# Optimization experiments

Measured on AMD Instinct MI355X. Metric: run time of the kernel, lower is better.

Reference implementation:

```python
import jax, jax.numpy as jnp
import numpy as np

# dims matching init_kwargs
B, N = 1, 2048
VOCAB, DIM, DEPTH = 32000, 1024, 4
HEADS, DIM_HEAD, WINDOW = 16, 64, 512
INNER = HEADS * DIM_HEAD          # 1024
FF_INNER = int(DIM * 4 * 2 / 3)   # 2730 (GEGLU inner)
DPB_DIM = DIM // 2
LN_EPS = 1e-5


def layernorm(x, g, b):
    m = jnp.mean(x, axis=-1, keepdims=True)
    v = jnp.mean(jnp.square(x - m), axis=-1, keepdims=True)
    return (x - m) * jax.lax.rsqrt(v + LN_EPS) * g + b


def look_around(x, backward=1, forward=0, pad_value=-1):
    # x: [b, nw, w, ...]; concat shifted windows along the window_size axis
    nw = x.shape[1]
    pads = [(0, 0), (backward, forward)] + [(0, 0)] * (x.ndim - 2)
    px = jnp.pad(x, pads, constant_values=pad_value)
    return jnp.concatenate([px[:, i:i + nw] for i in range(backward + forward + 1)], axis=2)


def dynamic_pos_bias(w1, b1, w2, b2, w3, b3, i, j):
    # MLP over scalar relative distances, then gather into [H, i, j]
    rel = jnp.arange(j, dtype=jnp.float32)[:, None]            # [j, 1]
    h = jax.nn.silu(rel @ w1 + b1)
    h = jax.nn.silu(h @ w2 + b2)
    bias = h @ w3 + b3                                          # [j, H]
    idx = jnp.abs(jnp.arange(j - i, j)[:, None] - jnp.arange(j)[None, :])  # [i, j]
    return jnp.transpose(bias[idx], (2, 0, 1))                  # [H, i, j]


def local_attention(q, k, v, attn_bias):
    # causal sliding-window attention, look_backward=1, look_forward=0, exact_windowsize=True
    # q,k,v: [B,H,N,dh]; N assumed multiple of WINDOW (autopad is a no-op then)
    b, h, n, d = q.shape
    w = WINDOW
    nw = n // w
    scale = d ** -0.5
    bq = q.reshape(b * h, nw, w, d) * scale
    bk = look_around(k.reshape(b * h, nw, w, d), pad_value=-1.0)   # [bh,nw,2w,d]
    bv = look_around(v.reshape(b * h, nw, w, d), pad_value=-1.0)
    t = jnp.arange(n).reshape(1, nw, w)
    bq_t = t[..., :, None]                                      # [1,nw,w,1]
    bq_k = look_around(t, pad_value=-1)[..., None, :]           # [1,nw,1,2w]
    # causal | exact-window | padding masks
    mask = (bq_t < bq_k) | (bq_t > bq_k + w) | (bq_k == -1)
    sim = jnp.einsum('bwid,bwjd->bwij', bq, bk)                 # [bh,nw,w,2w]
    sim = (sim.reshape(b, h, nw, w, 2 * w) + attn_bias[None, :, None]).reshape(b * h, nw, w, 2 * w)
    sim = jnp.where(mask, -jnp.finfo(sim.dtype).max, sim)
    attn = jax.nn.softmax(sim, axis=-1)
    out = jnp.einsum('bwij,bwjd->bwid', attn, bv)
    return out.reshape(b, h, n, d)


def forward(tokens, tok_emb, pos_emb, dpb_w1, dpb_b1, dpb_w2, dpb_b2, dpb_w3, dpb_b3,
            ln1_g, ln1_b, Wqkv, Wo, ln2_g, ln2_b, Wff1, Wff2, lnf_g, lnf_b, Wlogits):
    bsz, n = tokens.shape
    x = tok_emb[tokens] + pos_emb[:n]                           # [B,N,D]
    bias = dynamic_pos_bias(dpb_w1, dpb_b1, dpb_w2, dpb_b2, dpb_w3, dpb_b3, WINDOW, 2 * WINDOW)

    def split_heads(t):
        return t.reshape(bsz, n, HEADS, DIM_HEAD).transpose(0, 2, 1, 3)

    for l in range(DEPTH):
        # LocalMHA (prenorm) + residual
        h = layernorm(x, ln1_g[l], ln1_b[l])
        q, k, v = jnp.split(h @ Wqkv[l], 3, axis=-1)
        o = local_attention(split_heads(q), split_heads(k), split_heads(v), bias)
        o = o.transpose(0, 2, 1, 3).reshape(bsz, n, INNER)
        x = x + o @ Wo[l]
        # GEGLU FFN (prenorm inside FeedForward) + residual
        h = layernorm(x, ln2_g[l], ln2_b[l])
        a, gate = jnp.split(h @ Wff1[l], 2, axis=-1)
        x = x + (a * jax.nn.gelu(gate, approximate=False)) @ Wff2[l]

    return layernorm(x, lnf_g, lnf_b) @ Wlogits                 # [B,N,V]


def setup_inputs() -> dict:
    key = jax.random.key(0)
    ks = iter(jax.random.split(key, 16))
    s = 0.02
    rn = lambda *shape: jax.random.normal(next(ks), shape, dtype=jnp.float32) * s
    return {
        'tokens': jax.random.randint(next(ks), (B, N), 0, VOCAB, dtype=jnp.int32),
        'tok_emb': rn(VOCAB, DIM),
        'pos_emb': rn(N, DIM),
        'dpb_w1': rn(1, DPB_DIM), 'dpb_b1': jnp.zeros((DPB_DIM,), jnp.float32),
        'dpb_w2': rn(DPB_DIM, DPB_DIM), 'dpb_b2': jnp.zeros((DPB_DIM,), jnp.float32),
        'dpb_w3': rn(DPB_DIM, HEADS), 'dpb_b3': jnp.zeros((HEADS,), jnp.float32),
        'ln1_g': jnp.ones((DEPTH, DIM), jnp.float32), 'ln1_b': jnp.zeros((DEPTH, DIM), jnp.float32),
        'Wqkv': rn(DEPTH, DIM, 3 * INNER),
        'Wo': rn(DEPTH, INNER, DIM),
        'ln2_g': jnp.ones((DEPTH, DIM), jnp.float32), 'ln2_b': jnp.zeros((DEPTH, DIM), jnp.float32),
        'Wff1': rn(DEPTH, DIM, 2 * FF_INNER),
        'Wff2': rn(DEPTH, FF_INNER, DIM),
        'lnf_g': jnp.ones((DIM,), jnp.float32), 'lnf_b': jnp.zeros((DIM,), jnp.float32),
        'Wlogits': rn(DIM, VOCAB),
    }


def reference(tokens, tok_emb, pos_emb, dpb_w1, dpb_b1, dpb_w2, dpb_b2, dpb_w3, dpb_b3,
              ln1_g, ln1_b, Wqkv, Wo, ln2_g, ln2_b, Wff1, Wff2, lnf_g, lnf_b, Wlogits):
    return forward(tokens, tok_emb, pos_emb, dpb_w1, dpb_b1, dpb_w2, dpb_b2, dpb_w3, dpb_b3,
                   ln1_g, ln1_b, Wqkv, Wo, ln2_g, ln2_b, Wff1, Wff2, lnf_g, lnf_b, Wlogits)
```

## Files before the change

### kernel.cpp

```cpp
#include <hip/hip_runtime.h>
#include <cstdint>

#define DEV __device__ __forceinline__

typedef __attribute__((ext_vector_type(8))) short bf16x8;
typedef __attribute__((ext_vector_type(4))) short bf16x4;
typedef __attribute__((ext_vector_type(4))) float f32x4;

DEV float bf2f(unsigned short u) { return __uint_as_float(((unsigned)u) << 16); }
DEV unsigned short f2bf(float f) {
  unsigned u = __float_as_uint(f);
  u += 0x7FFFu + ((u >> 16) & 1u);
  return (unsigned short)(u >> 16);
}

DEV void gload_lds16(const void* g, void* lds) {
  __builtin_amdgcn_global_load_lds(
      (const __attribute__((address_space(1))) unsigned int*)g,
      (__attribute__((address_space(3))) unsigned int*)lds, 16, 0, 0);
}

__global__ __launch_bounds__(256) void k_embed(const int* __restrict__ tokens,
    const float* __restrict__ tok_emb, const float* __restrict__ pos_emb,
    float* __restrict__ x) {
  int n = blockIdx.x;
  int tok = tokens[n];
  int c = threadIdx.x * 4;
  float4 a = *(const float4*)(tok_emb + (long)tok * 1024 + c);
  float4 p = *(const float4*)(pos_emb + (long)n * 1024 + c);
  float4 r;
  r.x = a.x + p.x; r.y = a.y + p.y; r.z = a.z + p.z; r.w = a.w + p.w;
  *(float4*)(x + (long)n * 1024 + c) = r;
}

__global__ __launch_bounds__(256) void k_ln(const float* __restrict__ x,
    const float* __restrict__ g, const float* __restrict__ b,
    unsigned short* __restrict__ out) {
  __shared__ float red[8];
  int row = blockIdx.x, t = threadIdx.x;
  const float* xr = x + (long)row * 1024;
  float4 v = *(const float4*)(xr + t * 4);
  float s = v.x + v.y + v.z + v.w;
#pragma unroll
  for (int off = 32; off; off >>= 1) s += __shfl_xor(s, off);
  if ((t & 63) == 0) red[t >> 6] = s;
  __syncthreads();
  float mean = (red[0] + red[1] + red[2] + red[3]) * (1.0f / 1024.0f);
  float dx = v.x - mean, dy = v.y - mean, dz = v.z - mean, dw = v.w - mean;
  float sq = dx * dx + dy * dy + dz * dz + dw * dw;
#pragma unroll
  for (int off = 32; off; off >>= 1) sq += __shfl_xor(sq, off);
  if ((t & 63) == 0) red[4 + (t >> 6)] = sq;
  __syncthreads();
  float var = (red[4] + red[5] + red[6] + red[7]) * (1.0f / 1024.0f);
  float inv = rsqrtf(var + 1e-5f);
  int c = t * 4;
  float4 gv = *(const float4*)(g + c);
  float4 bv = *(const float4*)(b + c);
  ushort4 o;
  o.x = f2bf(dx * inv * gv.x + bv.x);
  o.y = f2bf(dy * inv * gv.y + bv.y);
  o.z = f2bf(dz * inv * gv.z + bv.z);
  o.w = f2bf(dw * inv * gv.w + bv.w);
  *(ushort4*)(out + (long)row * 1024 + c) = o;
}

__global__ __launch_bounds__(256) void k_wconv(const float* __restrict__ src,
    unsigned short* __restrict__ dst, int K, int N, int Kp, int Np,
    long sstride, long dstride) {
  __shared__ float tile[32][33];
  const float* s = src + (long)blockIdx.z * sstride;
  unsigned short* d = dst + (long)blockIdx.z * dstride;
  int n0 = blockIdx.x * 32, k0 = blockIdx.y * 32;
  int t = threadIdx.x;
  int r = t >> 3, c4 = (t & 7) * 4;
  int k = k0 + r;
#pragma unroll
  for (int e = 0; e < 4; ++e) {
    int n = n0 + c4 + e;
    tile[r][c4 + e] = (k < K && n < N) ? s[(long)k * N + n] : 0.0f;
  }
  __syncthreads();
  int nrow = n0 + r;
  ushort4 o;
  o.x = f2bf(tile[c4 + 0][r]);
  o.y = f2bf(tile[c4 + 1][r]);
  o.z = f2bf(tile[c4 + 2][r]);
  o.w = f2bf(tile[c4 + 3][r]);
  (void)Np;
  *(ushort4*)(d + (long)nrow * Kp + k0 + c4) = o;
}

__global__ __launch_bounds__(256) void k_dpb(const float* __restrict__ w1,
    const float* __restrict__ b1, const float* __restrict__ w2,
    const float* __restrict__ b2, const float* __restrict__ w3,
    const float* __restrict__ b3, float* __restrict__ table) {
  __shared__ float h1[512], h2[512];
  int r = blockIdx.x, t = threadIdx.x;
  float rf = (float)r;
  for (int c = t; c < 512; c += 256) {
    float v = rf * w1[c] + b1[c];
    h1[c] = v / (1.0f + __expf(-v));
  }
  __syncthreads();
  for (int c = t; c < 512; c += 256) {
    float acc = b2[c];
    for (int k2 = 0; k2 < 512; ++k2) acc = fmaf(h1[k2], w2[(long)k2 * 512 + c], acc);
    h2[c] = acc / (1.0f + __expf(-acc));
  }
  __syncthreads();
  if (t < 16) {
    float acc = b3[t];
    for (int k2 = 0; k2 < 512; ++k2) acc = fmaf(h2[k2], w3[k2 * 16 + t], acc);
    table[r * 16 + t] = acc;
  }
}

__global__ __launch_bounds__(256) void k_glu(const unsigned short* __restrict__ ff,
    unsigned short* __restrict__ u) {
  int row = blockIdx.x, t = threadIdx.x;
  const unsigned short* fr = ff + (long)row * 5504;
  unsigned short* ur = u + (long)row * 2752;
  for (int c = t; c < 2752; c += 256) {
    float val = 0.0f;
    if (c < 2730) {
      float a = bf2f(fr[c]);
      float gt = bf2f(fr[2730 + c]);
      val = a * (0.5f * gt * (1.0f + erff(gt * 0.70710678118654752f)));
    }
    ur[c] = f2bf(val);
  }
}

__global__ __launch_bounds__(256, 2) void k_attn_mfma(
    const unsigned short* __restrict__ qkv, const float* __restrict__ table,
    unsigned short* __restrict__ o) {
  __shared__ unsigned short Ks[64 * 64];
  __shared__ unsigned short Vt[64 * 72];
  __shared__ unsigned short Ps[4][16 * 72];
  __shared__ float biasl[1024];
  const int qt = blockIdx.x, h = blockIdx.y, wi = blockIdx.z;
  const int iw0 = qt * 64;
  const int t = threadIdx.x;
  const int w = t >> 6, l = t & 63;
  const int lq = l & 15, lk = l >> 4;

  for (int i = t; i < 1024; i += 256) biasl[i] = table[i * 16 + h];

  const unsigned short* qp = qkv + (long)(wi * 512 + iw0 + w * 16 + lq) * 3072 + h * 64;
  bf16x8 qf0 = *(const bf16x8*)(qp + lk * 8);
  bf16x8 qf1 = *(const bf16x8*)(qp + 32 + lk * 8);

  f32x4 oacc[4] = {};
  float mrun[4] = {-3.0e38f, -3.0e38f, -3.0e38f, -3.0e38f};
  float srun[4] = {};

  const int kt0 = (wi == 0) ? 8 : qt;
  const int kt1 = qt + 8;
  for (int kt = kt0; kt <= kt1; ++kt) {
    const int ktbase = kt * 64;
    const long kgbase = (long)((wi - 1) * 512 + ktbase);
    __syncthreads();
    {
      const unsigned short* Kg = qkv + kgbase * 3072 + 1024 + h * 64;
#pragma unroll
      for (int s2 = 0; s2 < 2; ++s2) {
        int g = s2 * 4 + w;
        int row = g * 8 + (l >> 3);
        int gch = (l & 7) ^ (row & 7);
        gload_lds16(Kg + (long)row * 3072 + gch * 8, &Ks[g * 512]);
      }
    }
    {
      int kp = t & 31, dg = t >> 5;
      const unsigned short* Vg =
          qkv + (kgbase + 2 * kp) * 3072 + 2048 + h * 64 + dg * 8;
      bf16x8 a0 = *(const bf16x8*)Vg;
      bf16x8 a1 = *(const bf16x8*)(Vg + 3072);
#pragma unroll
      for (int e = 0; e < 8; ++e) {
        unsigned pack = ((unsigned)(unsigned short)a0[e]) |
                        (((unsigned)(unsigned short)a1[e]) << 16);
        *(unsigned*)&Vt[(dg * 8 + e) * 72 + 2 * kp] = pack;
      }
    }
    asm volatile("s_waitcnt vmcnt(0)" ::: "memory");
    __syncthreads();

    f32x4 sacc[4] = {};
#pragma unroll
    for (int ct = 0; ct < 4; ++ct) {
      int krow = ct * 16 + lq;
      bf16x8 kf0 = *(const bf16x8*)&Ks[krow * 64 + (((0 + lk) ^ (krow & 7)) * 8)];
      bf16x8 kf1 = *(const bf16x8*)&Ks[krow * 64 + (((4 + lk) ^ (krow & 7)) * 8)];
      sacc[ct] = __builtin_amdgcn_mfma_f32_16x16x32_bf16(qf0, kf0, sacc[ct], 0, 0, 0);
      sacc[ct] = __builtin_amdgcn_mfma_f32_16x16x32_bf16(qf1, kf1, sacc[ct], 0, 0, 0);
    }

#pragma unroll
    for (int r = 0; r < 4; ++r) {
      const int iw = iw0 + w * 16 + lk * 4 + r;
      float sc[4];
#pragma unroll
      for (int ct = 0; ct < 4; ++ct) {
        int jj = ktbase + ct * 16 + lq;
        int di = 512 + iw - jj;
        int dic = min(max(di, 0), 1023);
        bool allowed = (jj >= iw) && (jj <= iw + 512);
        float v = sacc[ct][r] * 0.125f + biasl[dic];
        sc[ct] = allowed ? v : -3.0e38f;
      }
      float mx = fmaxf(fmaxf(sc[0], sc[1]), fmaxf(sc[2], sc[3]));
      mx = fmaxf(mx, __shfl_xor(mx, 1));
      mx = fmaxf(mx, __shfl_xor(mx, 2));
      mx = fmaxf(mx, __shfl_xor(mx, 4));
      mx = fmaxf(mx, __shfl_xor(mx, 8));
      float mnew = fmaxf(mrun[r], mx);
      float f = __expf(mrun[r] - mnew);
      mrun[r] = mnew;
      float rs = 0.0f;
#pragma unroll
      for (int ct = 0; ct < 4; ++ct) {
        float pv = __expf(sc[ct] - mnew);
        rs += pv;
        Ps[w][(lk * 4 + r) * 72 + ct * 16 + lq] = f2bf(pv);
      }
      rs += __shfl_xor(rs, 1);
      rs += __shfl_xor(rs, 2);
      rs += __shfl_xor(rs, 4);
      rs += __shfl_xor(rs, 8);
      srun[r] = srun[r] * f + rs;
#pragma unroll
      for (int dt = 0; dt < 4; ++dt) oacc[dt][r] *= f;
    }
    asm volatile("s_waitcnt lgkmcnt(0)" ::: "memory");

#pragma unroll
    for (int ks = 0; ks < 2; ++ks) {
      bf16x4 pa0 = *(const bf16x4*)&Ps[w][lq * 72 + ks * 32 + lk * 8];
      bf16x4 pa1 = *(const bf16x4*)&Ps[w][lq * 72 + ks * 32 + lk * 8 + 4];
      bf16x8 pa = __builtin_shufflevector(pa0, pa1, 0, 1, 2, 3, 4, 5, 6, 7);
#pragma unroll
      for (int dt = 0; dt < 4; ++dt) {
        int drow = dt * 16 + lq;
        bf16x4 vb0 = *(const bf16x4*)&Vt[drow * 72 + ks * 32 + lk * 8];
        bf16x4 vb1 = *(const bf16x4*)&Vt[drow * 72 + ks * 32 + lk * 8 + 4];
        bf16x8 vb = __builtin_shufflevector(vb0, vb1, 0, 1, 2, 3, 4, 5, 6, 7);
        oacc[dt] = __builtin_amdgcn_mfma_f32_16x16x32_bf16(pa, vb, oacc[dt], 0, 0, 0);
      }
    }
  }

  unsigned short* ob =
      o + (long)(wi * 512 + iw0 + w * 16 + lk * 4) * 1024 + h * 64 + lq;
#pragma unroll
  for (int r = 0; r < 4; ++r) {
    float inv = 1.0f / srun[r];
#pragma unroll
    for (int dt = 0; dt < 4; ++dt)
      ob[(long)r * 1024 + dt * 16] = f2bf(oacc[dt][r] * inv);
  }
}

template <int EPI>
__global__ __launch_bounds__(256, 2) void k_gemm(const unsigned short* __restrict__ A,
    const unsigned short* __restrict__ BT, void* __restrict__ Cout,
    int M, int N, int K) {
  __shared__ unsigned short As[128 * 64];
  __shared__ unsigned short Bs[128 * 64];
  const int bn = blockIdx.x, bm = blockIdx.y;
  const int t = threadIdx.x;
  const int w = t >> 6, l = t & 63;
  const int wm = w >> 1, wn = w & 1;
  const int lrow = l >> 3, lch = l & 7;
  const int lq = l & 15, lk = l >> 4;
  f32x4 acc[4][4] = {};
  const long arow0 = (long)bm * 128, brow0 = (long)bn * 128;
  for (int kt = 0; kt < K; kt += 64) {
    __syncthreads();
#pragma unroll
    for (int s2 = 0; s2 < 4; ++s2) {
      int grp = s2 * 4 + w;
      int r = grp * 8 + lrow;
      int gch = lch ^ lrow;
      gload_lds16(A + (arow0 + r) * K + kt + gch * 8, &As[grp * 512]);
      gload_lds16(BT + (brow0 + r) * K + kt + gch * 8, &Bs[grp * 512]);
    }
    asm volatile("s_waitcnt vmcnt(0)" ::: "memory");
    __syncthreads();
#pragma unroll
    for (int kk = 0; kk < 2; ++kk) {
      bf16x8 af[4], bfr[4];
#pragma unroll
      for (int i = 0; i < 4; ++i) {
        int ra = wm * 64 + i * 16 + lq;
        af[i] = *(const bf16x8*)&As[ra * 64 + (((kk * 4 + lk) ^ (ra & 7)) * 8)];
        int rb = wn * 64 + i * 16 + lq;
        bfr[i] = *(const bf16x8*)&Bs[rb * 64 + (((kk * 4 + lk) ^ (rb & 7)) * 8)];
      }
#pragma unroll
      for (int i = 0; i < 4; ++i)
#pragma unroll
        for (int j = 0; j < 4; ++j)
          acc[i][j] = __builtin_amdgcn_mfma_f32_16x16x32_bf16(af[i], bfr[j],
                                                              acc[i][j], 0, 0, 0);
    }
  }
  (void)M;
  const int rbase = bm * 128 + wm * 64 + lk * 4;
  const int cbase = bn * 128 + wn * 64 + lq;
#pragma unroll
  for (int i = 0; i < 4; ++i) {
#pragma unroll
    for (int j = 0; j < 4; ++j) {
#pragma unroll
      for (int r2 = 0; r2 < 4; ++r2) {
        long row = rbase + i * 16 + r2;
        long col = cbase + j * 16;
        float v = acc[i][j][r2];
        if (EPI == 0)
          ((unsigned short*)Cout)[row * N + col] = f2bf(v);
        else if (EPI == 1)
          ((float*)Cout)[row * N + col] += v;
        else
          ((float*)Cout)[row * N + col] = v;
      }
    }
  }
}

extern "C" void kernel_launch(void* const* d_in, const int* in_sizes, int n_in,
                              void* d_out, int out_size, void* d_ws, size_t ws_size,
                              hipStream_t stream) {
  (void)in_sizes; (void)n_in; (void)out_size; (void)ws_size;
  const int* tokens   = (const int*)d_in[0];
  const float* tok_emb = (const float*)d_in[1];
  const float* pos_emb = (const float*)d_in[2];
  const float* dpb_w1 = (const float*)d_in[3];
  const float* dpb_b1 = (const float*)d_in[4];
  const float* dpb_w2 = (const float*)d_in[5];
  const float* dpb_b2 = (const float*)d_in[6];
  const float* dpb_w3 = (const float*)d_in[7];
  const float* dpb_b3 = (const float*)d_in[8];
  const float* ln1_g  = (const float*)d_in[9];
  const float* ln1_b  = (const float*)d_in[10];
  const float* Wqkv   = (const float*)d_in[11];
  const float* Wo     = (const float*)d_in[12];
  const float* ln2_g  = (const float*)d_in[13];
  const float* ln2_b  = (const float*)d_in[14];
  const float* Wff1   = (const float*)d_in[15];
  const float* Wff2   = (const float*)d_in[16];
  const float* lnf_g  = (const float*)d_in[17];
  const float* lnf_b  = (const float*)d_in[18];
  const float* Wlog   = (const float*)d_in[19];
  float* out = (float*)d_out;

  char* p = (char*)d_ws;
  auto carve = [&](size_t bytes) {
    char* q = p;
    p += (bytes + 255) & ~(size_t)255;
    return (void*)q;
  };
  unsigned short* WqkvT = (unsigned short*)carve((size_t)4 * 3072 * 1024 * 2);
  unsigned short* WoT   = (unsigned short*)carve((size_t)4 * 1024 * 1024 * 2);
  unsigned short* Wff1T = (unsigned short*)carve((size_t)4 * 5504 * 1024 * 2);
  unsigned short* Wff2T = (unsigned short*)carve((size_t)4 * 1024 * 2752 * 2);
  unsigned short* WlogT = (unsigned short*)carve((size_t)32000 * 1024 * 2);
  float*          x     = (float*)carve((size_t)2048 * 1024 * 4);
  unsigned short* hbuf  = (unsigned short*)carve((size_t)2048 * 1024 * 2);
  unsigned short* qkv   = (unsigned short*)carve((size_t)2048 * 3072 * 2);
  unsigned short* ao    = (unsigned short*)carve((size_t)2048 * 1024 * 2);
  unsigned short* ff    = (unsigned short*)carve((size_t)2048 * 5504 * 2);
  unsigned short* ubuf  = (unsigned short*)carve((size_t)2048 * 2752 * 2);
  float*          table = (float*)carve((size_t)1024 * 16 * 4);

  k_wconv<<<dim3(3072 / 32, 1024 / 32, 4), 256, 0, stream>>>(
      Wqkv, WqkvT, 1024, 3072, 1024, 3072, (long)1024 * 3072, (long)3072 * 1024);
  k_wconv<<<dim3(1024 / 32, 1024 / 32, 4), 256, 0, stream>>>(
      Wo, WoT, 1024, 1024, 1024, 1024, (long)1024 * 1024, (long)1024 * 1024);
  k_wconv<<<dim3(5504 / 32, 1024 / 32, 4), 256, 0, stream>>>(
      Wff1, Wff1T, 1024, 5460, 1024, 5504, (long)1024 * 5460, (long)5504 * 1024);
  k_wconv<<<dim3(1024 / 32, 2752 / 32, 4), 256, 0, stream>>>(
      Wff2, Wff2T, 2730, 1024, 2752, 1024, (long)2730 * 1024, (long)1024 * 2752);
  k_wconv<<<dim3(32000 / 32, 1024 / 32, 1), 256, 0, stream>>>(
      Wlog, WlogT, 1024, 32000, 1024, 32000, 0L, 0L);

  k_dpb<<<1024, 256, 0, stream>>>(dpb_w1, dpb_b1, dpb_w2, dpb_b2, dpb_w3, dpb_b3, table);
  k_embed<<<2048, 256, 0, stream>>>(tokens, tok_emb, pos_emb, x);

  for (int l = 0; l < 4; ++l) {
    k_ln<<<2048, 256, 0, stream>>>(x, ln1_g + l * 1024, ln1_b + l * 1024, hbuf);
    k_gemm<0><<<dim3(3072 / 128, 16), 256, 0, stream>>>(
        hbuf, WqkvT + (long)l * 3072 * 1024, qkv, 2048, 3072, 1024);
    k_attn_mfma<<<dim3(8, 16, 4), 256, 0, stream>>>(qkv, table, ao);
    k_gemm<1><<<dim3(1024 / 128, 16), 256, 0, stream>>>(
        ao, WoT + (long)l * 1024 * 1024, x, 2048, 1024, 1024);
    k_ln<<<2048, 256, 0, stream>>>(x, ln2_g + l * 1024, ln2_b + l * 1024, hbuf);
    k_gemm<0><<<dim3(5504 / 128, 16), 256, 0, stream>>>(
        hbuf, Wff1T + (long)l * 5504 * 1024, ff, 2048, 5504, 1024);
    k_glu<<<2048, 256, 0, stream>>>(ff, ubuf);
    k_gemm<1><<<dim3(1024 / 128, 16), 256, 0, stream>>>(
        ubuf, Wff2T + (long)l * 1024 * 2752, x, 2048, 1024, 2752);
  }
  k_ln<<<2048, 256, 0, stream>>>(x, lnf_g, lnf_b, hbuf);
  k_gemm<2><<<dim3(32000 / 128, 16), 256, 0, stream>>>(
      hbuf, WlogT, out, 2048, 32000, 1024);
}
```

Measured before the change: 1.235 ms.

## Remap GEMM workgroups per XCD and vectorize weight-convert and GEGLU kernels

GEMM launches switch from a 2D grid to a 1D grid. The workgroup id is remapped so that consecutive tiles, with the M index varying fastest, land on the same XCD. The aim is for blocks sharing a B column tile to hit the same L2 instead of spreading across the 8 XCD caches. The weight conversion kernel now loads float4 instead of four scalar loads, and the GEGLU kernel processes four elements per thread with vector loads and stores. This adds index arithmetic per block and depends on round-robin XCD dispatch of workgroups.

```diff
diff --git a/kernel.cpp b/kernel.cpp
--- a/kernel.cpp
+++ b/kernel.cpp
@@ -74,12 +74,13 @@
   int n0 = blockIdx.x * 32, k0 = blockIdx.y * 32;
   int t = threadIdx.x;
   int r = t >> 3, c4 = (t & 7) * 4;
-  int k = k0 + r;
-#pragma unroll
-  for (int e = 0; e < 4; ++e) {
-    int n = n0 + c4 + e;
-    tile[r][c4 + e] = (k < K && n < N) ? s[(long)k * N + n] : 0.0f;
-  }
+  int k = k0 + r, n = n0 + c4;
+  float4 v = make_float4(0.f, 0.f, 0.f, 0.f);
+  if (k < K && n < N) v = *(const float4*)(s + (long)k * N + n);
+  tile[r][c4 + 0] = v.x;
+  tile[r][c4 + 1] = v.y;
+  tile[r][c4 + 2] = v.z;
+  tile[r][c4 + 3] = v.w;
   __syncthreads();
   int nrow = n0 + r;
   ushort4 o;
@@ -121,14 +122,22 @@
   int row = blockIdx.x, t = threadIdx.x;
   const unsigned short* fr = ff + (long)row * 5504;
   unsigned short* ur = u + (long)row * 2752;
-  for (int c = t; c < 2752; c += 256) {
-    float val = 0.0f;
-    if (c < 2730) {
-      float a = bf2f(fr[c]);
-      float gt = bf2f(fr[2730 + c]);
-      val = a * (0.5f * gt * (1.0f + erff(gt * 0.70710678118654752f)));
-    }
-    ur[c] = f2bf(val);
+  for (int c = t * 4; c < 2752; c += 1024) {
+    ushort4 av = *(const ushort4*)(fr + c);
+    ushort2 g0 = *(const ushort2*)(fr + 2730 + c);
+    ushort2 g1 = *(const ushort2*)(fr + 2730 + c + 2);
+    float aa[4] = {bf2f(av.x), bf2f(av.y), bf2f(av.z), bf2f(av.w)};
+    float gg[4] = {bf2f(g0.x), bf2f(g0.y), bf2f(g1.x), bf2f(g1.y)};
+    ushort4 o;
+    unsigned short* op = (unsigned short*)&o;
+#pragma unroll
+    for (int e = 0; e < 4; ++e) {
+      float val = 0.0f;
+      if (c + e < 2730)
+        val = aa[e] * (0.5f * gg[e] * (1.0f + erff(gg[e] * 0.70710678118654752f)));
+      op[e] = f2bf(val);
+    }
+    *(ushort4*)(ur + c) = o;
   }
 }
 
@@ -265,10 +274,16 @@
 template <int EPI>
 __global__ __launch_bounds__(256, 2) void k_gemm(const unsigned short* __restrict__ A,
     const unsigned short* __restrict__ BT, void* __restrict__ Cout,
-    int M, int N, int K) {
+    int N, int K, int nbm) {
   __shared__ unsigned short As[128 * 64];
   __shared__ unsigned short Bs[128 * 64];
-  const int bn = blockIdx.x, bm = blockIdx.y;
+  const int nwg = gridDim.x;
+  const int orig = blockIdx.x;
+  const int q8 = nwg >> 3, r8 = nwg & 7;
+  const int xcd = orig & 7, i8 = orig >> 3;
+  const int wgid = (xcd < r8 ? xcd * (q8 + 1) : r8 * (q8 + 1) + (xcd - r8) * q8) + i8;
+  const int bm = wgid % nbm;
+  const int bn = wgid / nbm;
   const int t = threadIdx.x;
   const int w = t >> 6, l = t & 63;
   const int wm = w >> 1, wn = w & 1;
@@ -306,7 +321,6 @@
                                                               acc[i][j], 0, 0, 0);
     }
   }
-  (void)M;
   const int rbase = bm * 128 + wm * 64 + lk * 4;
   const int cbase = bn * 128 + wn * 64 + lq;
 #pragma unroll
@@ -388,21 +402,22 @@
   k_dpb<<<1024, 256, 0, stream>>>(dpb_w1, dpb_b1, dpb_w2, dpb_b2, dpb_w3, dpb_b3, table);
   k_embed<<<2048, 256, 0, stream>>>(tokens, tok_emb, pos_emb, x);
 
+  const int NBM = 16;
   for (int l = 0; l < 4; ++l) {
     k_ln<<<2048, 256, 0, stream>>>(x, ln1_g + l * 1024, ln1_b + l * 1024, hbuf);
-    k_gemm<0><<<dim3(3072 / 128, 16), 256, 0, stream>>>(
-        hbuf, WqkvT + (long)l * 3072 * 1024, qkv, 2048, 3072, 1024);
+    k_gemm<0><<<dim3(NBM * (3072 / 128)), 256, 0, stream>>>(
+        hbuf, WqkvT + (long)l * 3072 * 1024, qkv, 3072, 1024, NBM);
     k_attn_mfma<<<dim3(8, 16, 4), 256, 0, stream>>>(qkv, table, ao);
-    k_gemm<1><<<dim3(1024 / 128, 16), 256, 0, stream>>>(
-        ao, WoT + (long)l * 1024 * 1024, x, 2048, 1024, 1024);
+    k_gemm<1><<<dim3(NBM * (1024 / 128)), 256, 0, stream>>>(
+        ao, WoT + (long)l * 1024 * 1024, x, 1024, 1024, NBM);
     k_ln<<<2048, 256, 0, stream>>>(x, ln2_g + l * 1024, ln2_b + l * 1024, hbuf);
-    k_gemm<0><<<dim3(5504 / 128, 16), 256, 0, stream>>>(
-        hbuf, Wff1T + (long)l * 5504 * 1024, ff, 2048, 5504, 1024);
+    k_gemm<0><<<dim3(NBM * (5504 / 128)), 256, 0, stream>>>(
+        hbuf, Wff1T + (long)l * 5504 * 1024, ff, 5504, 1024, NBM);
     k_glu<<<2048, 256, 0, stream>>>(ff, ubuf);
-    k_gemm<1><<<dim3(1024 / 128, 16), 256, 0, stream>>>(
-        ubuf, Wff2T + (long)l * 1024 * 2752, x, 2048, 1024, 2752);
+    k_gemm<1><<<dim3(NBM * (1024 / 128)), 256, 0, stream>>>(
+        ubuf, Wff2T + (long)l * 1024 * 2752, x, 1024, 2752, NBM);
   }
   k_ln<<<2048, 256, 0, stream>>>(x, lnf_g, lnf_b, hbuf);
-  k_gemm<2><<<dim3(32000 / 128, 16), 256, 0, stream>>>(
-      hbuf, WlogT, out, 2048, 32000, 1024);
-}
+  k_gemm<2><<<dim3(NBM * (32000 / 128)), 256, 0, stream>>>(
+      hbuf, WlogT, out, 32000, 1024, NBM);
+}
```

Result: faster. 1.183 ms (-4.2%).
